# Kernel optimization log

Measured on AMD Instinct MI355X. Metric: run time of the kernel, lower is better.

## Reference

```python
import jax, jax.numpy as jnp
import numpy as np


def setup_inputs() -> dict:
    key = jax.random.key(0)
    ks = jax.random.split(key, 10)
    N, CZ, CH = 512, 128, 128
    s = 1.0 / np.sqrt(CZ)  # keep pre-sigmoid activations in a sane range
    return {
        "z": jax.random.normal(ks[0], (N, N, CZ), dtype=jnp.float32),
        "mask": jnp.ones((N, N, 1), dtype=jnp.float32),
        "weight_ag": jax.random.normal(ks[1], (CH, CZ), dtype=jnp.float32) * s,
        "bias_ag": jax.random.normal(ks[2], (CH,), dtype=jnp.float32) * 0.02,
        "weight_ap": jax.random.normal(ks[3], (CH, CZ), dtype=jnp.float32) * s,
        "bias_ap": jax.random.normal(ks[4], (CH,), dtype=jnp.float32) * 0.02,
        "weight_bg": jax.random.normal(ks[5], (CH, CZ), dtype=jnp.float32) * s,
        "bias_bg": jax.random.normal(ks[6], (CH,), dtype=jnp.float32) * 0.02,
        "weight_bp": jax.random.normal(ks[7], (CH, CZ), dtype=jnp.float32) * s,
        "bias_bp": jax.random.normal(ks[8], (CH,), dtype=jnp.float32) * 0.02,
        "chunk_size": 32,
    }


def _triangle_mul(z, mask, w_ag, b_ag, w_ap, b_ap, w_bg, b_bg, w_bp, b_bp):
    # z: [N, N, c_z]; mask: [N, N, 1]; weights: [c, c_z]
    # a = mask * sigmoid(Linear_ag(z)) * Linear_ap(z)   -> [N, N, c]
    a = mask * jax.nn.sigmoid(jnp.einsum("ijz,cz->ijc", z, w_ag) + b_ag) * (
        jnp.einsum("ijz,cz->ijc", z, w_ap) + b_ap
    )
    b = mask * jax.nn.sigmoid(jnp.einsum("ijz,cz->ijc", z, w_bg) + b_bg) * (
        jnp.einsum("ijz,cz->ijc", z, w_bp) + b_bp
    )
    # outgoing triangle multiplicative combination, channel-first output [c, N, N]
    return jnp.einsum("ikc,jkc->cij", a, b)


def reference(z, mask, weight_ag, bias_ag, weight_ap, bias_ap,
              weight_bg, bias_bg, weight_bp, bias_bp, chunk_size):
    # The torch wrapper chunks the hidden-channel dim of the weights and
    # concatenates the per-chunk [c, N, N] outputs along dim 0. Since every
    # channel is independent, this is mathematically identical to running the
    # full computation at once; we do that (clean, fused form).
    return _triangle_mul(z, mask, weight_ag, bias_ag, weight_ap, bias_ap,
                         weight_bg, bias_bg, weight_bp, bias_bp)
```

## Files before the change

### kernel.cpp

```cpp
#include <hip/hip_runtime.h>
#include <stdint.h>


#define NDIM 512
#define CZ   128
#define CH   128
#define NPOS (NDIM * NDIM)
#define NTILE 8
#define POSB  (NTILE * 32)

typedef __attribute__((ext_vector_type(8))) __bf16 bf16x8;
typedef __attribute__((ext_vector_type(4))) float  f32x4;

__device__ __forceinline__ unsigned short f2bf(float f) {
  unsigned int u = __builtin_bit_cast(unsigned int, f);
  unsigned int r = (u + 0x7fffu + ((u >> 16) & 1u)) >> 16;
  return (unsigned short)r;
}
__device__ __forceinline__ unsigned int cvt_pk_bf16(float lo, float hi) {
  unsigned int r;
  asm("v_cvt_pk_bf16_f32 %0, %1, %2" : "=v"(r) : "v"(lo), "v"(hi));
  return r;
}

__global__ __launch_bounds__(256) void conv_weights(
    const float* __restrict__ wag, const float* __restrict__ wap,
    const float* __restrict__ wbg, const float* __restrict__ wbp,
    unsigned short* __restrict__ wbf) {
  int idx = blockIdx.x * 256 + threadIdx.x;
  int proj = idx >> 14;
  int rem  = idx & 16383;
  const float* src = (proj == 0) ? wag : (proj == 1) ? wap : (proj == 2) ? wbg : wbp;
  wbf[idx] = f2bf(src[rem]);
}

__global__ __launch_bounds__(256, 3) void proj_fuse(
    const float* __restrict__ z,
    const float* __restrict__ mask,
    const unsigned short* __restrict__ wbf,
    const float* __restrict__ bias_ag, const float* __restrict__ bias_ap,
    const float* __restrict__ bias_bg, const float* __restrict__ bias_bp,
    unsigned short* __restrict__ a_ws,
    unsigned short* __restrict__ b_ws) {
  __shared__ unsigned short zbuf[2][32 * 136];

  const int t    = threadIdx.x;
  const int lane = t & 63;
  const int w    = t >> 6;
  const int pair = blockIdx.y;
  const int base = blockIdx.x * POSB;

  const int ml    = lane & 15;
  const int q     = lane >> 4;
  const int koffl = q * 8;
  const int pg = pair * 2, pp = pg + 1;

  bf16x8 wg[4][2], wp[4][2];
#pragma unroll
  for (int ks = 0; ks < 4; ++ks)
#pragma unroll
    for (int ni = 0; ni < 2; ++ni) {
      const int c = w * 32 + ni * 16 + ml;
      wg[ks][ni] = *(const bf16x8*)&wbf[((size_t)pg * CH + c) * CZ + ks * 32 + koffl];
      wp[ks][ni] = *(const bf16x8*)&wbf[((size_t)pp * CH + c) * CZ + ks * 32 + koffl];
    }
#pragma unroll
  for (int ks = 0; ks < 4; ++ks)
#pragma unroll
    for (int ni = 0; ni < 2; ++ni) {
      asm volatile("" : "+v"(wg[ks][ni]));
      asm volatile("" : "+v"(wp[ks][ni]));
    }

  const float* bgp = pair ? bias_bg : bias_ag;
  const float* bpp = pair ? bias_bp : bias_ap;
  float bg[2], bp[2];
#pragma unroll
  for (int ni = 0; ni < 2; ++ni) {
    bg[ni] = bgp[w * 32 + ni * 16 + ml];
    bp[ni] = bpp[w * 32 + ni * 16 + ml];
  }
  unsigned short* plane = pair ? b_ws : a_ws;

  float4 stg[4];
  auto STAGE_LOAD = [&](int tt) {
    const int m0s = base + tt * 32;
#pragma unroll
    for (int it = 0; it < 4; ++it) {
      const int id  = it * 256 + t;
      stg[it] = *(const float4*)(z + (size_t)(m0s + (id >> 5)) * CZ + (id & 31) * 4);
    }
  };
  auto STAGE_WRITE = [&](int b) {
#pragma unroll
    for (int it = 0; it < 4; ++it) {
      const int id = it * 256 + t;
      *(uint2*)&zbuf[b][(id >> 5) * 136 + (id & 31) * 4] =
          make_uint2(cvt_pk_bf16(stg[it].x, stg[it].y),
                     cvt_pk_bf16(stg[it].z, stg[it].w));
    }
  };

  STAGE_LOAD(0);
  STAGE_WRITE(0);
  __syncthreads();

#pragma unroll 1
  for (int tt = 0; tt < NTILE; ++tt) {
    const int m0 = base + tt * 32;
    const int cb = tt & 1;
    if (tt + 1 < NTILE) STAGE_LOAD(tt + 1);

    f32x4 ag_[2][2], ap_[2][2];
#pragma unroll
    for (int mi = 0; mi < 2; ++mi)
#pragma unroll
      for (int ni = 0; ni < 2; ++ni) {
        ag_[mi][ni] = (f32x4){0.f, 0.f, 0.f, 0.f};
        ap_[mi][ni] = (f32x4){0.f, 0.f, 0.f, 0.f};
      }

#pragma unroll
    for (int ks = 0; ks < 4; ++ks) {
      bf16x8 af0 = *(const bf16x8*)&zbuf[cb][(ml)      * 136 + ks * 32 + koffl];
      bf16x8 af1 = *(const bf16x8*)&zbuf[cb][(ml + 16) * 136 + ks * 32 + koffl];
#pragma unroll
      for (int ni = 0; ni < 2; ++ni) {
        ag_[0][ni] = __builtin_amdgcn_mfma_f32_16x16x32_bf16(af0, wg[ks][ni], ag_[0][ni], 0, 0, 0);
        ag_[1][ni] = __builtin_amdgcn_mfma_f32_16x16x32_bf16(af1, wg[ks][ni], ag_[1][ni], 0, 0, 0);
        ap_[0][ni] = __builtin_amdgcn_mfma_f32_16x16x32_bf16(af0, wp[ks][ni], ap_[0][ni], 0, 0, 0);
        ap_[1][ni] = __builtin_amdgcn_mfma_f32_16x16x32_bf16(af1, wp[ks][ni], ap_[1][ni], 0, 0, 0);
      }
    }

#pragma unroll
    for (int mi = 0; mi < 2; ++mi) {
      const int pos0 = mi * 16 + q * 4;
      const float4 mv = *(const float4*)(mask + m0 + pos0);
      const float mr[4] = {mv.x, mv.y, mv.z, mv.w};
#pragma unroll
      for (int ni = 0; ni < 2; ++ni) {
        const int c = w * 32 + ni * 16 + ml;
        float v[4];
#pragma unroll
        for (int r = 0; r < 4; ++r) {
          const float g = ag_[mi][ni][r] + bg[ni];
          const float p = ap_[mi][ni][r] + bp[ni];
          const float s = __builtin_amdgcn_rcpf(1.0f + __expf(-g));
          v[r] = mr[r] * s * p;
        }
        *(uint2*)(plane + (size_t)c * NPOS + m0 + pos0) =
            make_uint2(cvt_pk_bf16(v[0], v[1]), cvt_pk_bf16(v[2], v[3]));
      }
    }

    if (tt + 1 < NTILE) STAGE_WRITE(cb ^ 1);
    __syncthreads();
  }
}

__global__ __launch_bounds__(512) void tri_gemm(
    const unsigned short* __restrict__ a_ws,
    const unsigned short* __restrict__ b_ws,
    float* __restrict__ out) {
  __shared__ unsigned short sA[2][256 * 64];
  __shared__ unsigned short sB[2][256 * 64];

  const int t = threadIdx.x, lane = t & 63, wave = t >> 6;
  const int wm = wave >> 2;
  const int wn = wave & 3;

  const int L    = blockIdx.x;
  const int xcd  = L & 7;
  const int slot = L >> 3;
  const int c    = xcd * 16 + (slot >> 2);
  const int tile = slot & 3;
  const int ti   = tile >> 1, tj = tile & 1;
  const int i0 = ti * 256, j0 = tj * 256;

  const unsigned short* Ap = a_ws + (size_t)c * NPOS + (size_t)i0 * NDIM;
  const unsigned short* Bp = b_ws + (size_t)c * NPOS + (size_t)j0 * NDIM;

  f32x4 acc[8][4];
#pragma unroll
  for (int mi = 0; mi < 8; ++mi)
#pragma unroll
    for (int ni = 0; ni < 4; ++ni) acc[mi][ni] = (f32x4){0.f, 0.f, 0.f, 0.f};

  const int srow   = t >> 3;
  const int schunk = t & 7;
  const int mrow = wm * 128 + (lane & 15);
  const int nrow = wn * 64 + (lane & 15);

  auto STAGE = [&](int b, int kk) {
    const int k0 = kk * 64;
#pragma unroll
    for (int i = 0; i < 4; ++i) {
      const int row = i * 64 + srow;
      const int kcs = schunk ^ (row & 7);
      __builtin_amdgcn_global_load_lds(
          (const __attribute__((address_space(1))) unsigned int*)(Ap + (size_t)row * NDIM + k0 + kcs * 8),
          (__attribute__((address_space(3))) unsigned int*)&sA[b][(i * 512 + t) * 8], 16, 0, 0);
      __builtin_amdgcn_global_load_lds(
          (const __attribute__((address_space(1))) unsigned int*)(Bp + (size_t)row * NDIM + k0 + kcs * 8),
          (__attribute__((address_space(3))) unsigned int*)&sB[b][(i * 512 + t) * 8], 16, 0, 0);
    }
  };

  auto COMPUTE = [&](int cur) {
#pragma unroll
    for (int ksub = 0; ksub < 2; ++ksub) {
      const int kc = ksub * 4 + (lane >> 4);
      bf16x8 af[8], bfr[4];
#pragma unroll
      for (int mi = 0; mi < 8; ++mi) {
        const int r = mrow + mi * 16;
        af[mi] = *(const bf16x8*)&sA[cur][r * 64 + ((kc ^ (r & 7)) << 3)];
      }
#pragma unroll
      for (int ni = 0; ni < 4; ++ni) {
        const int r = nrow + ni * 16;
        bfr[ni] = *(const bf16x8*)&sB[cur][r * 64 + ((kc ^ (r & 7)) << 3)];
      }
#pragma unroll
      for (int mi = 0; mi < 8; ++mi)
#pragma unroll
        for (int ni = 0; ni < 4; ++ni)
          acc[mi][ni] = __builtin_amdgcn_mfma_f32_16x16x32_bf16(af[mi], bfr[ni], acc[mi][ni], 0, 0, 0);
    }
  };

  STAGE(0, 0);

#pragma unroll 1
  for (int kk = 0; kk < 7; ++kk) {
    const int cur = kk & 1;
    STAGE(cur ^ 1, kk + 1);
    asm volatile("s_waitcnt vmcnt(8)" ::: "memory");
    __builtin_amdgcn_s_barrier();
    COMPUTE(cur);
    __builtin_amdgcn_s_barrier();
  }
  asm volatile("s_waitcnt vmcnt(0)" ::: "memory");
  __builtin_amdgcn_s_barrier();
  COMPUTE(1);

  float* O = out + (size_t)c * NPOS + (size_t)i0 * NDIM + j0;
#pragma unroll
  for (int mi = 0; mi < 8; ++mi)
#pragma unroll
    for (int r = 0; r < 4; ++r) {
      const int m = wm * 128 + mi * 16 + (lane >> 4) * 4 + r;
#pragma unroll
      for (int ni = 0; ni < 4; ++ni) {
        const int n = wn * 64 + ni * 16 + (lane & 15);
        O[(size_t)m * NDIM + n] = acc[mi][ni][r];
      }
    }
}

extern "C" void kernel_launch(void* const* d_in, const int* in_sizes, int n_in,
                              void* d_out, int out_size, void* d_ws, size_t ws_size,
                              hipStream_t stream) {
  const float* z    = (const float*)d_in[0];
  const float* mask = (const float*)d_in[1];
  const float* wag  = (const float*)d_in[2];
  const float* bag  = (const float*)d_in[3];
  const float* wap  = (const float*)d_in[4];
  const float* bap  = (const float*)d_in[5];
  const float* wbg  = (const float*)d_in[6];
  const float* bbg  = (const float*)d_in[7];
  const float* wbp  = (const float*)d_in[8];
  const float* bbp  = (const float*)d_in[9];
  float* out = (float*)d_out;

  unsigned short* wbf  = (unsigned short*)d_ws;
  unsigned short* a_ws = (unsigned short*)((char*)d_ws + 131072);
  unsigned short* b_ws = (unsigned short*)((char*)d_ws + 131072 + (size_t)CH * NPOS * 2);

  conv_weights<<<dim3(256), dim3(256), 0, stream>>>(wag, wap, wbg, wbp, wbf);
  proj_fuse<<<dim3(NPOS / POSB, 2), dim3(256), 0, stream>>>(
      z, mask, wbf, bag, bap, bbg, bbp, a_ws, b_ws);
  tri_gemm<<<dim3(512), dim3(512), 0, stream>>>(a_ws, b_ws, out);
}
```

Baseline: 362.4 us.

## Stage z tiles via direct global-to-LDS loads with triple buffering

The projection kernel now loads fp32 z tiles straight into shared memory with global_load_lds into a 3-deep ring buffer, using an XOR swizzle to avoid bank conflicts. Conversion to bf16 moves from the staging write to the point where the MFMA operands are read. This removes the register round-trip for staging and lets two tiles of loads stay in flight, at the cost of twice the LDS per tile (fp32 instead of bf16), which may lower occupancy. Synchronisation now relies on hand-written vmcnt waits and raw barriers, which makes correctness depend on exact load counts.

```diff
diff --git a/kernel.cpp b/kernel.cpp
--- a/kernel.cpp
+++ b/kernel.cpp
@@ -11,6 +11,7 @@
 
 typedef __attribute__((ext_vector_type(8))) __bf16 bf16x8;
 typedef __attribute__((ext_vector_type(4))) float  f32x4;
+typedef __attribute__((ext_vector_type(4))) unsigned int u32x4;
 
 __device__ __forceinline__ unsigned short f2bf(float f) {
   unsigned int u = __builtin_bit_cast(unsigned int, f);
@@ -21,6 +22,11 @@
   unsigned int r;
   asm("v_cvt_pk_bf16_f32 %0, %1, %2" : "=v"(r) : "v"(lo), "v"(hi));
   return r;
+}
+__device__ __forceinline__ bf16x8 pack8(float4 lo, float4 hi) {
+  u32x4 u = {cvt_pk_bf16(lo.x, lo.y), cvt_pk_bf16(lo.z, lo.w),
+             cvt_pk_bf16(hi.x, hi.y), cvt_pk_bf16(hi.z, hi.w)};
+  return __builtin_bit_cast(bf16x8, u);
 }
 
 __global__ __launch_bounds__(256) void conv_weights(
@@ -42,7 +48,7 @@
     const float* __restrict__ bias_bg, const float* __restrict__ bias_bp,
     unsigned short* __restrict__ a_ws,
     unsigned short* __restrict__ b_ws) {
-  __shared__ unsigned short zbuf[2][32 * 136];
+  __shared__ float zb[3][32 * 128];
 
   const int t    = threadIdx.x;
   const int lane = t & 63;
@@ -52,8 +58,9 @@
 
   const int ml    = lane & 15;
   const int q     = lane >> 4;
+  const int mlm   = ml & 7;
+  const int pg = pair * 2, pp = pg + 1;
   const int koffl = q * 8;
-  const int pg = pair * 2, pp = pg + 1;
 
   bf16x8 wg[4][2], wp[4][2];
 #pragma unroll
@@ -82,34 +89,26 @@
   }
   unsigned short* plane = pair ? b_ws : a_ws;
 
-  float4 stg[4];
-  auto STAGE_LOAD = [&](int tt) {
+  auto STAGE = [&](int b, int tt) {
     const int m0s = base + tt * 32;
 #pragma unroll
-    for (int it = 0; it < 4; ++it) {
-      const int id  = it * 256 + t;
-      stg[it] = *(const float4*)(z + (size_t)(m0s + (id >> 5)) * CZ + (id & 31) * 4);
+    for (int i = 0; i < 4; ++i) {
+      const int n     = i * 256 + t;
+      const int row   = n >> 5;
+      const int pch   = n & 31;
+      const int sch   = pch ^ (row & 7);
+      __builtin_amdgcn_global_load_lds(
+          (const __attribute__((address_space(1))) unsigned int*)(
+              z + (size_t)(m0s + row) * CZ + sch * 4),
+          (__attribute__((address_space(3))) unsigned int*)&zb[b][n * 4],
+          16, 0, 0);
     }
   };
-  auto STAGE_WRITE = [&](int b) {
-#pragma unroll
-    for (int it = 0; it < 4; ++it) {
-      const int id = it * 256 + t;
-      *(uint2*)&zbuf[b][(id >> 5) * 136 + (id & 31) * 4] =
-          make_uint2(cvt_pk_bf16(stg[it].x, stg[it].y),
-                     cvt_pk_bf16(stg[it].z, stg[it].w));
-    }
-  };
-
-  STAGE_LOAD(0);
-  STAGE_WRITE(0);
-  __syncthreads();
-
-#pragma unroll 1
-  for (int tt = 0; tt < NTILE; ++tt) {
+
+  auto TILE = [&](int tt, int b) {
     const int m0 = base + tt * 32;
-    const int cb = tt & 1;
-    if (tt + 1 < NTILE) STAGE_LOAD(tt + 1);
+    const float* Zr0 = &zb[b][ml * 128];
+    const float* Zr1 = &zb[b][(ml + 16) * 128];
 
     f32x4 ag_[2][2], ap_[2][2];
 #pragma unroll
@@ -122,8 +121,13 @@
 
 #pragma unroll
     for (int ks = 0; ks < 4; ++ks) {
-      bf16x8 af0 = *(const bf16x8*)&zbuf[cb][(ml)      * 136 + ks * 32 + koffl];
-      bf16x8 af1 = *(const bf16x8*)&zbuf[cb][(ml + 16) * 136 + ks * 32 + koffl];
+      const int jp = (ks * 8 + q * 2) ^ mlm;
+      const float4 a0l = *(const float4*)(Zr0 + ((jp)     << 2));
+      const float4 a0h = *(const float4*)(Zr0 + ((jp ^ 1) << 2));
+      const float4 a1l = *(const float4*)(Zr1 + ((jp)     << 2));
+      const float4 a1h = *(const float4*)(Zr1 + ((jp ^ 1) << 2));
+      const bf16x8 af0 = pack8(a0l, a0h);
+      const bf16x8 af1 = pack8(a1l, a1h);
 #pragma unroll
       for (int ni = 0; ni < 2; ++ni) {
         ag_[0][ni] = __builtin_amdgcn_mfma_f32_16x16x32_bf16(af0, wg[ks][ni], ag_[0][ni], 0, 0, 0);
@@ -153,10 +157,26 @@
             make_uint2(cvt_pk_bf16(v[0], v[1]), cvt_pk_bf16(v[2], v[3]));
       }
     }
-
-    if (tt + 1 < NTILE) STAGE_WRITE(cb ^ 1);
-    __syncthreads();
+  };
+
+  STAGE(0, 0);
+  STAGE(1, 1);
+
+#pragma unroll 1
+  for (int tt = 0; tt < NTILE - 2; ++tt) {
+    STAGE((tt + 2) % 3, tt + 2);
+    asm volatile("s_waitcnt vmcnt(8)" ::: "memory");
+    __builtin_amdgcn_s_barrier();
+    TILE(tt, tt % 3);
+    __builtin_amdgcn_s_barrier();
   }
+  asm volatile("s_waitcnt vmcnt(4)" ::: "memory");
+  __builtin_amdgcn_s_barrier();
+  TILE(NTILE - 2, (NTILE - 2) % 3);
+  __builtin_amdgcn_s_barrier();
+  asm volatile("s_waitcnt vmcnt(0)" ::: "memory");
+  __builtin_amdgcn_s_barrier();
+  TILE(NTILE - 1, (NTILE - 1) % 3);
 }
 
 __global__ __launch_bounds__(512) void tri_gemm(
```

Result: slower. 383.0 us (+5.7%).
